# Optimization experiments

Hardware: AMD Instinct MI355X
Metric: run time of the kernel (lower is better)

## Reference

```python
import jax, jax.numpy as jnp
import numpy as np

E = 32      # particle_embed_dim = q/k/v head out dim
G = 2       # nof_net_types (conv groups)
NEG_SLOPE = 0.01


def _glin(x, w, b, groups):
    """Grouped 1x1 conv on (M, C, 1, 1) == grouped linear.
    x: (M, Cin), w: (Cout, Cin//groups), b: (Cout,)."""
    M = x.shape[0]
    Cout = w.shape[0]
    xg = x.reshape(M, groups, -1)                 # (M, G, Cin/G)
    wg = w.reshape(groups, Cout // groups, -1)    # (G, Cout/G, Cin/G)
    y = jnp.einsum('mgi,goi->mgo', xg, wg).reshape(M, Cout)
    return y + b


def setup_inputs() -> dict:
    key = jax.random.key(0)
    ks = jax.random.split(key, 9)
    B, N = 32, 1024
    s = 0.05
    return {
        'x_e':   jax.random.normal(ks[0], (B, N, G * E), dtype=jnp.float32),
        'w_qkv': jax.random.normal(ks[1], (3 * G * E, E), dtype=jnp.float32) * s,
        'b_qkv': jax.random.normal(ks[2], (3 * G * E,), dtype=jnp.float32) * s,
        'w_h1':  jax.random.normal(ks[3], (G * E, 2 * E), dtype=jnp.float32) * s,
        'b_h1':  jax.random.normal(ks[4], (G * E,), dtype=jnp.float32) * s,
        'w_h10': jax.random.normal(ks[5], (G * E, E), dtype=jnp.float32) * s,
        'b_h10': jax.random.normal(ks[6], (G * E,), dtype=jnp.float32) * s,
        'w_h11': jax.random.normal(ks[7], (G * E, E), dtype=jnp.float32) * s,
        'b_h11': jax.random.normal(ks[8], (G * E,), dtype=jnp.float32) * s,
    }


def reference(x_e, w_qkv, b_qkv, w_h1, b_h1, w_h10, b_h10, w_h11, b_h11):
    B, N, D = x_e.shape                      # D = G*E = 64
    act = lambda z: jnp.where(z >= 0, z, NEG_SLOPE * z)

    # grouped 1x1-conv QKV projection
    qkv = _glin(x_e.reshape(B * N, D), w_qkv, b_qkv, G)        # (B*N, 3*G*E)
    qkv = qkv.reshape(B, N, G, 3, E).transpose(0, 2, 3, 1, 4)  # (B, G, 3, N, E)
    q, k, v = qkv[:, :, 0], qkv[:, :, 1], qkv[:, :, 2]         # each (B, G, N, E)

    # NOTE: module divides k by sqrt(E) and logits by sqrt(E) again -> 1/E total
    scale = 1.0 / E
    ip = jnp.einsum('bgne,bgme->bgnm', q, k) * scale           # (B, G, N, N)
    sip = jax.nn.softmax(ip, axis=-1)
    attn = jnp.einsum('bgnm,bgme->bgne', sip, v)               # (B, G, N, E)

    # concat pre-attention v with attention output, regroup per-particle
    x_xe = jnp.concatenate([v, attn], axis=3)                  # (B, G, N, 2E)
    x_xe = x_xe.transpose(0, 2, 1, 3).reshape(B * N, G * 2 * E)  # (B*N, 128)

    h = act(_glin(x_xe, w_h1, b_h1, G))
    h = act(_glin(h, w_h10, b_h10, G))
    h = act(_glin(h, w_h11, b_h11, G))
    return h.reshape(B * N, G * E, 1, 1)
```

## Files before the change

kernel.cpp:

```cpp
#include <hip/hip_runtime.h>

#define B_ 32
#define N_ 1024
#define NEG 0.01f
#define QSC (1.4426950408889634f/32.0f)

using half8  = __attribute__((ext_vector_type(8))) _Float16;
using half4  = __attribute__((ext_vector_type(4))) _Float16;
using half2  = __attribute__((ext_vector_type(2))) _Float16;
using fp16x2 = __attribute__((ext_vector_type(2))) __fp16;
using floatx4 = __attribute__((ext_vector_type(4))) float;

#if defined(__has_builtin)
#if __has_builtin(__builtin_amdgcn_exp2f)
#define EXP2(x) __builtin_amdgcn_exp2f(x)
#endif
#endif
#ifndef EXP2
#define EXP2(x) exp2f(x)
#endif

__device__ inline half2 pkcvt(float a, float b) {
    fp16x2 r = __builtin_amdgcn_cvt_pkrtz(a, b);
    return __builtin_bit_cast(half2, r);
}

__device__ inline half8 cvt8(float4 a, float4 b) {
    half2 p0 = pkcvt(a.x, a.y);
    half2 p1 = pkcvt(a.z, a.w);
    half2 p2 = pkcvt(b.x, b.y);
    half2 p3 = pkcvt(b.z, b.w);
    half8 h = { p0[0],p0[1], p1[0],p1[1], p2[0],p2[1], p3[0],p3[1] };
    return h;
}

struct __align__(16) Smem {
    _Float16 wsh[96*36];
    float    bsh[96];
    _Float16 Kst[2][128*40];
    _Float16 Vtst[2][32*136];
    union {
        _Float16 qs[128*40];
        _Float16 xs[128*72];
    } u;
    float linv[128];
    float bl1[32], bl10[32], bl11[32];
};

__global__ __launch_bounds__(256, 2) void fused_kernel(
    const float* __restrict__ x, const float* __restrict__ w_qkv, const float* __restrict__ b_qkv,
    const float* __restrict__ w_h1,  const float* __restrict__ b_h1,
    const float* __restrict__ w_h10, const float* __restrict__ b_h10,
    const float* __restrict__ w_h11, const float* __restrict__ b_h11,
    float* __restrict__ out)
{
    __shared__ Smem sm;
    int t = threadIdx.x;
    int bg = blockIdx.x >> 3;
    int qtile = blockIdx.x & 7;
    int b = bg >> 1, g = bg & 1;
    int qbase = qtile * 128;
    int lane = t & 63, w = t >> 6;
    int L15 = lane & 15, quad = lane >> 4;

    for (int idx = t; idx < 96*32; idx += 256) {
        int r = idx >> 5, c = idx & 31;
        float wv = w_qkv[(g*96 + r)*32 + c];
        sm.wsh[r*36 + c] = (_Float16)(r < 32 ? wv*QSC : wv);
    }
    if (t < 96) sm.bsh[t] = b_qkv[g*96 + t];
    if (t < 32) {
        sm.bl1[t]  = b_h1[g*32+t];
        sm.bl10[t] = b_h10[g*32+t];
        sm.bl11[t] = b_h11[g*32+t];
    }
    __syncthreads();

    half8 bwq[2], bwk[2], bwv[2];
    floatx4 cq[2], ck[2], cv[2];
    #pragma unroll
    for (int et = 0; et < 2; et++) {
        bwq[et] = *(const half8*)&sm.wsh[(     et*16 + L15)*36 + quad*8];
        bwk[et] = *(const half8*)&sm.wsh[(32 + et*16 + L15)*36 + quad*8];
        bwv[et] = *(const half8*)&sm.wsh[(64 + et*16 + L15)*36 + quad*8];
        float bq = sm.bsh[     et*16 + L15] * QSC;
        float bk = sm.bsh[32 + et*16 + L15];
        float bv = sm.bsh[64 + et*16 + L15];
        cq[et] = (floatx4){bq,bq,bq,bq};
        ck[et] = (floatx4){bk,bk,bk,bk};
        cv[et] = (floatx4){bv,bv,bv,bv};
    }

    {
        floatx4 dq[2][2];
        #pragma unroll
        for (int mt = 0; mt < 2; mt++) {
            const float* p = x + ((size_t)b*N_ + qbase + w*32 + mt*16 + L15)*64 + g*32 + quad*8;
            half8 axq = cvt8(*(const float4*)p, *(const float4*)(p + 4));
            dq[mt][0] = __builtin_amdgcn_mfma_f32_16x16x32_f16(axq, bwq[0], cq[0], 0,0,0);
            dq[mt][1] = __builtin_amdgcn_mfma_f32_16x16x32_f16(axq, bwq[1], cq[1], 0,0,0);
        }
        #pragma unroll
        for (int mt = 0; mt < 2; mt++)
            #pragma unroll
            for (int et = 0; et < 2; et++)
                #pragma unroll
                for (int r = 0; r < 4; r++)
                    sm.u.qs[(w*32 + mt*16 + quad*4 + r)*40 + et*16 + L15] =
                        (_Float16)dq[mt][et][r];
    }
    __syncthreads();
    half8 bq0 = *(const half8*)&sm.u.qs[(w*32 +      L15)*40 + quad*8];
    half8 bq1 = *(const half8*)&sm.u.qs[(w*32 + 16 + L15)*40 + quad*8];

    float4 xf0[2], xf1[2];
    auto prefetch = [&](int tile) {
        #pragma unroll
        for (int mt = 0; mt < 2; mt++) {
            const float* p = x + ((size_t)b*N_ + tile*128 + w*32 + mt*16 + L15)*64 + g*32 + quad*8;
            xf0[mt] = *(const float4*)p;
            xf1[mt] = *(const float4*)(p + 4);
        }
    };
    auto proj_tile = [&](int tile, int buf) {
        floatx4 dK[2][2], dV[2][2];
        #pragma unroll
        for (int mt = 0; mt < 2; mt++) {
            half8 axk = cvt8(xf0[mt], xf1[mt]);
            dK[mt][0] = __builtin_amdgcn_mfma_f32_16x16x32_f16(axk, bwk[0], ck[0], 0,0,0);
            dK[mt][1] = __builtin_amdgcn_mfma_f32_16x16x32_f16(axk, bwk[1], ck[1], 0,0,0);
            dV[mt][0] = __builtin_amdgcn_mfma_f32_16x16x32_f16(axk, bwv[0], cv[0], 0,0,0);
            dV[mt][1] = __builtin_amdgcn_mfma_f32_16x16x32_f16(axk, bwv[1], cv[1], 0,0,0);
        }
        #pragma unroll
        for (int mt = 0; mt < 2; mt++) {
            int rb = w*32 + mt*16 + quad*4;
            #pragma unroll
            for (int et = 0; et < 2; et++) {
                half2 k01 = pkcvt(dK[mt][et][0], dK[mt][et][1]);
                half2 k23 = pkcvt(dK[mt][et][2], dK[mt][et][3]);
                half2 v01 = pkcvt(dV[mt][et][0], dV[mt][et][1]);
                half2 v23 = pkcvt(dV[mt][et][2], dV[mt][et][3]);
                half4 vh = { v01[0], v01[1], v23[0], v23[1] };
                sm.Kst[buf][(rb+0)*40 + et*16 + L15] = k01[0];
                sm.Kst[buf][(rb+1)*40 + et*16 + L15] = k01[1];
                sm.Kst[buf][(rb+2)*40 + et*16 + L15] = k23[0];
                sm.Kst[buf][(rb+3)*40 + et*16 + L15] = k23[1];
                *(half4*)&sm.Vtst[buf][(et*16 + L15)*136 + rb] = vh;
                if (tile == qtile) {
                    #pragma unroll
                    for (int r = 0; r < 4; r++)
                        sm.u.xs[(rb + r)*72 + et*16 + L15] = vh[r];
                }
            }
        }
    };

    prefetch(0);
    proj_tile(0, 0);
    __syncthreads();

    floatx4 o00 = {0.f,0.f,0.f,0.f}, o01 = o00, o10 = o00, o11 = o00;
    float lsum0 = 0.f, lsum1 = 0.f;

    for (int kt = 0; kt < 8; kt++) {
        int cur = kt & 1;
        if (kt < 7) prefetch(kt + 1);
        #pragma unroll
        for (int mt8 = 0; mt8 < 8; mt8++) {
            half8 ak = *(const half8*)&sm.Kst[cur][(mt8*16 + L15)*40 + quad*8];
            floatx4 zz = {0.f,0.f,0.f,0.f};
            floatx4 s0 = __builtin_amdgcn_mfma_f32_16x16x32_f16(ak, bq0, zz, 0,0,0);
            floatx4 s1 = __builtin_amdgcn_mfma_f32_16x16x32_f16(ak, bq1, zz, 0,0,0);
            float p00 = EXP2(s0.x), p01 = EXP2(s0.y), p02 = EXP2(s0.z), p03 = EXP2(s0.w);
            float p10 = EXP2(s1.x), p11 = EXP2(s1.y), p12 = EXP2(s1.z), p13 = EXP2(s1.w);
            lsum0 += (p00+p01)+(p02+p03);
            lsum1 += (p10+p11)+(p12+p13);
            half2 pa = pkcvt(p00, p01);
            half2 pb = pkcvt(p02, p03);
            half2 pc = pkcvt(p10, p11);
            half2 pd = pkcvt(p12, p13);
            half4 a0 = { pa[0], pa[1], pb[0], pb[1] };
            half4 a1 = { pc[0], pc[1], pd[0], pd[1] };
            half4 bv0 = *(const half4*)&sm.Vtst[cur][      L15*136 + mt8*16 + quad*4];
            half4 bv1 = *(const half4*)&sm.Vtst[cur][(16 + L15)*136 + mt8*16 + quad*4];
            o00 = __builtin_amdgcn_mfma_f32_16x16x16f16(a0, bv0, o00, 0,0,0);
            o01 = __builtin_amdgcn_mfma_f32_16x16x16f16(a0, bv1, o01, 0,0,0);
            o10 = __builtin_amdgcn_mfma_f32_16x16x16f16(a1, bv0, o10, 0,0,0);
            o11 = __builtin_amdgcn_mfma_f32_16x16x16f16(a1, bv1, o11, 0,0,0);
        }
        if (kt < 7) proj_tile(kt + 1, 1 - cur);
        __syncthreads();
    }

    lsum0 += __shfl_xor(lsum0, 16, 64); lsum0 += __shfl_xor(lsum0, 32, 64);
    lsum1 += __shfl_xor(lsum1, 16, 64); lsum1 += __shfl_xor(lsum1, 32, 64);
    if (quad == 0) {
        sm.linv[w*32 +      L15] = 1.0f / lsum0;
        sm.linv[w*32 + 16 + L15] = 1.0f / lsum1;
    }
    __syncthreads();

    {
        const floatx4* ofr[2][2] = { {&o00,&o01}, {&o10,&o11} };
        #pragma unroll
        for (int nt = 0; nt < 2; nt++) {
            float4 li = *(const float4*)&sm.linv[w*32 + nt*16 + quad*4];
            #pragma unroll
            for (int et = 0; et < 2; et++) {
                floatx4 ov = *ofr[nt][et];
                sm.u.xs[(w*32+nt*16+quad*4+0)*72 + 32 + et*16 + L15] = (_Float16)(ov[0]*li.x);
                sm.u.xs[(w*32+nt*16+quad*4+1)*72 + 32 + et*16 + L15] = (_Float16)(ov[1]*li.y);
                sm.u.xs[(w*32+nt*16+quad*4+2)*72 + 32 + et*16 + L15] = (_Float16)(ov[2]*li.z);
                sm.u.xs[(w*32+nt*16+quad*4+3)*72 + 32 + et*16 + L15] = (_Float16)(ov[3]*li.w);
            }
        }
    }
    __syncthreads();

    half4 a1f[2][4], a2f[2][2], a3f[2][2];
    #pragma unroll
    for (int mt = 0; mt < 2; mt++) {
        #pragma unroll
        for (int kt = 0; kt < 4; kt++) {
            float4 f = *(const float4*)(w_h1 + (size_t)(g*32+mt*16+L15)*64 + kt*16 + quad*4);
            half2 ha = pkcvt(f.x, f.y);
            half2 hb = pkcvt(f.z, f.w);
            half4 h = { ha[0], ha[1], hb[0], hb[1] };
            a1f[mt][kt] = h;
        }
        #pragma unroll
        for (int kt = 0; kt < 2; kt++) {
            float4 f = *(const float4*)(w_h10 + (size_t)(g*32+mt*16+L15)*32 + kt*16 + quad*4);
            half2 ha = pkcvt(f.x, f.y);
            half2 hb = pkcvt(f.z, f.w);
            half4 h = { ha[0], ha[1], hb[0], hb[1] };
            a2f[mt][kt] = h;
            float4 f2 = *(const float4*)(w_h11 + (size_t)(g*32+mt*16+L15)*32 + kt*16 + quad*4);
            half2 hc = pkcvt(f2.x, f2.y);
            half2 hd = pkcvt(f2.z, f2.w);
            half4 h2 = { hc[0], hc[1], hd[0], hd[1] };
            a3f[mt][kt] = h2;
        }
    }

    floatx4 d1[2][2];
    #pragma unroll
    for (int mt = 0; mt < 2; mt++) {
        float4 bb = *(const float4*)&sm.bl1[mt*16 + quad*4];
        floatx4 seed = { bb.x, bb.y, bb.z, bb.w };
        d1[mt][0] = seed; d1[mt][1] = seed;
    }
    #pragma unroll
    for (int nt = 0; nt < 2; nt++)
        #pragma unroll
        for (int kt = 0; kt < 4; kt++) {
            half4 b1 = *(const half4*)&sm.u.xs[(w*32+nt*16+L15)*72 + kt*16 + quad*4];
            d1[0][nt] = __builtin_amdgcn_mfma_f32_16x16x16f16(a1f[0][kt], b1, d1[0][nt], 0,0,0);
            d1[1][nt] = __builtin_amdgcn_mfma_f32_16x16x16f16(a1f[1][kt], b1, d1[1][nt], 0,0,0);
        }
    half4 h1b[2][2];
    #pragma unroll
    for (int mt = 0; mt < 2; mt++)
        #pragma unroll
        for (int nt = 0; nt < 2; nt++) {
            float v0 = d1[mt][nt][0]; v0 = (v0>=0.f)?v0:NEG*v0;
            float v1 = d1[mt][nt][1]; v1 = (v1>=0.f)?v1:NEG*v1;
            float v2 = d1[mt][nt][2]; v2 = (v2>=0.f)?v2:NEG*v2;
            float v3 = d1[mt][nt][3]; v3 = (v3>=0.f)?v3:NEG*v3;
            half2 ha = pkcvt(v0, v1);
            half2 hb = pkcvt(v2, v3);
            half4 h = { ha[0], ha[1], hb[0], hb[1] };
            h1b[mt][nt] = h;
        }
    floatx4 d2[2][2];
    #pragma unroll
    for (int mt = 0; mt < 2; mt++) {
        float4 bb = *(const float4*)&sm.bl10[mt*16 + quad*4];
        floatx4 seed = { bb.x, bb.y, bb.z, bb.w };
        d2[mt][0] = seed; d2[mt][1] = seed;
    }
    #pragma unroll
    for (int mt = 0; mt < 2; mt++)
        #pragma unroll
        for (int nt = 0; nt < 2; nt++)
            #pragma unroll
            for (int kt = 0; kt < 2; kt++)
                d2[mt][nt] = __builtin_amdgcn_mfma_f32_16x16x16f16(a2f[mt][kt], h1b[kt][nt], d2[mt][nt], 0,0,0);
    half4 h2b[2][2];
    #pragma unroll
    for (int mt = 0; mt < 2; mt++)
        #pragma unroll
        for (int nt = 0; nt < 2; nt++) {
            float v0 = d2[mt][nt][0]; v0 = (v0>=0.f)?v0:NEG*v0;
            float v1 = d2[mt][nt][1]; v1 = (v1>=0.f)?v1:NEG*v1;
            float v2 = d2[mt][nt][2]; v2 = (v2>=0.f)?v2:NEG*v2;
            float v3 = d2[mt][nt][3]; v3 = (v3>=0.f)?v3:NEG*v3;
            half2 ha = pkcvt(v0, v1);
            half2 hb = pkcvt(v2, v3);
            half4 h = { ha[0], ha[1], hb[0], hb[1] };
            h2b[mt][nt] = h;
        }
    floatx4 d3[2][2];
    #pragma unroll
    for (int mt = 0; mt < 2; mt++) {
        float4 bb = *(const float4*)&sm.bl11[mt*16 + quad*4];
        floatx4 seed = { bb.x, bb.y, bb.z, bb.w };
        d3[mt][0] = seed; d3[mt][1] = seed;
    }
    #pragma unroll
    for (int mt = 0; mt < 2; mt++)
        #pragma unroll
        for (int nt = 0; nt < 2; nt++)
            #pragma unroll
            for (int kt = 0; kt < 2; kt++)
                d3[mt][nt] = __builtin_amdgcn_mfma_f32_16x16x16f16(a3f[mt][kt], h2b[kt][nt], d3[mt][nt], 0,0,0);
    #pragma unroll
    for (int mt = 0; mt < 2; mt++)
        #pragma unroll
        for (int nt = 0; nt < 2; nt++) {
            float4 ov;
            ov.x = d3[mt][nt][0]; ov.x = (ov.x>=0.f)?ov.x:NEG*ov.x;
            ov.y = d3[mt][nt][1]; ov.y = (ov.y>=0.f)?ov.y:NEG*ov.y;
            ov.z = d3[mt][nt][2]; ov.z = (ov.z>=0.f)?ov.z:NEG*ov.z;
            ov.w = d3[mt][nt][3]; ov.w = (ov.w>=0.f)?ov.w:NEG*ov.w;
            *(float4*)(out + ((size_t)b*N_ + qbase + w*32 + nt*16 + L15)*64 + g*32 + mt*16 + quad*4) = ov;
        }
}

extern "C" void kernel_launch(void* const* d_in, const int* in_sizes, int n_in,
                              void* d_out, int out_size, void* d_ws, size_t ws_size,
                              hipStream_t stream) {
    const float* x_e   = (const float*)d_in[0];
    const float* w_qkv = (const float*)d_in[1];
    const float* b_qkv = (const float*)d_in[2];
    const float* w_h1  = (const float*)d_in[3];
    const float* b_h1  = (const float*)d_in[4];
    const float* w_h10 = (const float*)d_in[5];
    const float* b_h10 = (const float*)d_in[6];
    const float* w_h11 = (const float*)d_in[7];
    const float* b_h11 = (const float*)d_in[8];
    float* out = (float*)d_out;

    hipLaunchKernelGGL(fused_kernel, dim3(B_*2*8), dim3(256), 0, stream,
                       x_e, w_qkv, b_qkv, w_h1, b_h1, w_h10, b_h10, w_h11, b_h11, out);
}
```

Measured before the change: 98.32 us.

## Use 512-thread blocks with 16 query rows per wave and XCD-aware block mapping

Doubles the block to 8 waves so each wave owns 16 query rows instead of 32. This halves per-wave register state (one score MFMA per K subtile, two output accumulators) and raises occupancy through launch bounds 512,4. Block IDs are remapped so all query tiles of one batch-group land on the same XCD, improving L2 reuse of the shared K/V input. It also raises MFMA priority with s_setprio around the attention loop and replaces the shared-memory linv round-trip plus two barriers with wave shuffles. In exchange, the K/V projection is still recomputed per block and more waves contend at each barrier.

Result: slower. 150.2 us (+52.7%).

```diff
diff --git a/kernel.cpp b/kernel.cpp
--- a/kernel.cpp
+++ b/kernel.cpp
@@ -20,6 +20,9 @@
 #define EXP2(x) exp2f(x)
 #endif
 
+#define MFMA32 __builtin_amdgcn_mfma_f32_16x16x32_f16
+#define MFMA16 __builtin_amdgcn_mfma_f32_16x16x16f16
+
 __device__ inline half2 pkcvt(float a, float b) {
     fp16x2 r = __builtin_amdgcn_cvt_pkrtz(a, b);
     return __builtin_bit_cast(half2, r);
@@ -39,15 +42,12 @@
     float    bsh[96];
     _Float16 Kst[2][128*40];
     _Float16 Vtst[2][32*136];
-    union {
-        _Float16 qs[128*40];
-        _Float16 xs[128*72];
-    } u;
-    float linv[128];
+    _Float16 qs[128*40];
+    _Float16 xs[128*72];
     float bl1[32], bl10[32], bl11[32];
 };
 
-__global__ __launch_bounds__(256, 2) void fused_kernel(
+__global__ __launch_bounds__(512, 4) void fused_kernel(
     const float* __restrict__ x, const float* __restrict__ w_qkv, const float* __restrict__ b_qkv,
     const float* __restrict__ w_h1,  const float* __restrict__ b_h1,
     const float* __restrict__ w_h10, const float* __restrict__ b_h10,
@@ -56,14 +56,16 @@
 {
     __shared__ Smem sm;
     int t = threadIdx.x;
-    int bg = blockIdx.x >> 3;
-    int qtile = blockIdx.x & 7;
+    int bid = blockIdx.x;
+    int xcd = bid & 7, j = bid >> 3;
+    int bg = xcd*8 + (j >> 3);
+    int qtile = j & 7;
     int b = bg >> 1, g = bg & 1;
     int qbase = qtile * 128;
     int lane = t & 63, w = t >> 6;
     int L15 = lane & 15, quad = lane >> 4;
 
-    for (int idx = t; idx < 96*32; idx += 256) {
+    for (int idx = t; idx < 96*32; idx += 512) {
         int r = idx >> 5, c = idx & 31;
         float wv = w_qkv[(g*96 + r)*32 + c];
         sm.wsh[r*36 + c] = (_Float16)(r < 32 ? wv*QSC : wv);
@@ -76,82 +78,66 @@
     }
     __syncthreads();
 
-    half8 bwq[2], bwk[2], bwv[2];
-    floatx4 cq[2], ck[2], cv[2];
+    half8 bwk[2], bwv[2];
+    float bkv[2], bvv[2];
     #pragma unroll
     for (int et = 0; et < 2; et++) {
-        bwq[et] = *(const half8*)&sm.wsh[(     et*16 + L15)*36 + quad*8];
         bwk[et] = *(const half8*)&sm.wsh[(32 + et*16 + L15)*36 + quad*8];
         bwv[et] = *(const half8*)&sm.wsh[(64 + et*16 + L15)*36 + quad*8];
-        float bq = sm.bsh[     et*16 + L15] * QSC;
-        float bk = sm.bsh[32 + et*16 + L15];
-        float bv = sm.bsh[64 + et*16 + L15];
-        cq[et] = (floatx4){bq,bq,bq,bq};
-        ck[et] = (floatx4){bk,bk,bk,bk};
-        cv[et] = (floatx4){bv,bv,bv,bv};
+        bkv[et] = sm.bsh[32 + et*16 + L15];
+        bvv[et] = sm.bsh[64 + et*16 + L15];
     }
 
     {
-        floatx4 dq[2][2];
-        #pragma unroll
-        for (int mt = 0; mt < 2; mt++) {
-            const float* p = x + ((size_t)b*N_ + qbase + w*32 + mt*16 + L15)*64 + g*32 + quad*8;
-            half8 axq = cvt8(*(const float4*)p, *(const float4*)(p + 4));
-            dq[mt][0] = __builtin_amdgcn_mfma_f32_16x16x32_f16(axq, bwq[0], cq[0], 0,0,0);
-            dq[mt][1] = __builtin_amdgcn_mfma_f32_16x16x32_f16(axq, bwq[1], cq[1], 0,0,0);
-        }
-        #pragma unroll
-        for (int mt = 0; mt < 2; mt++)
+        const float* p = x + ((size_t)b*N_ + qbase + w*16 + L15)*64 + g*32 + quad*8;
+        half8 axq = cvt8(*(const float4*)p, *(const float4*)(p + 4));
+        #pragma unroll
+        for (int et = 0; et < 2; et++) {
+            half8 bwq = *(const half8*)&sm.wsh[(et*16 + L15)*36 + quad*8];
+            float bq = sm.bsh[et*16 + L15] * QSC;
+            floatx4 cq = {bq,bq,bq,bq};
+            floatx4 dq = MFMA32(axq, bwq, cq, 0,0,0);
             #pragma unroll
-            for (int et = 0; et < 2; et++)
+            for (int r = 0; r < 4; r++)
+                sm.qs[(w*16 + quad*4 + r)*40 + et*16 + L15] = (_Float16)dq[r];
+        }
+    }
+    __syncthreads();
+    half8 bq0 = *(const half8*)&sm.qs[(w*16 + L15)*40 + quad*8];
+
+    float4 xf0, xf1;
+    auto prefetch = [&](int tile) {
+        const float* p = x + ((size_t)b*N_ + tile*128 + w*16 + L15)*64 + g*32 + quad*8;
+        xf0 = *(const float4*)p;
+        xf1 = *(const float4*)(p + 4);
+    };
+    auto proj_tile = [&](int tile, int buf) {
+        half8 ax = cvt8(xf0, xf1);
+        floatx4 dK[2], dV[2];
+        #pragma unroll
+        for (int et = 0; et < 2; et++) {
+            floatx4 ck = {bkv[et],bkv[et],bkv[et],bkv[et]};
+            floatx4 cv = {bvv[et],bvv[et],bvv[et],bvv[et]};
+            dK[et] = MFMA32(ax, bwk[et], ck, 0,0,0);
+            dV[et] = MFMA32(ax, bwv[et], cv, 0,0,0);
+        }
+        int rb = w*16 + quad*4;
+        #pragma unroll
+        for (int et = 0; et < 2; et++) {
+            half2 k01 = pkcvt(dK[et][0], dK[et][1]);
+            half2 k23 = pkcvt(dK[et][2], dK[et][3]);
+            sm.Kst[buf][(rb+0)*40 + et*16 + L15] = k01[0];
+            sm.Kst[buf][(rb+1)*40 + et*16 + L15] = k01[1];
+            sm.Kst[buf][(rb+2)*40 + et*16 + L15] = k23[0];
+            sm.Kst[buf][(rb+3)*40 + et*16 + L15] = k23[1];
+            half2 v01 = pkcvt(dV[et][0], dV[et][1]);
+            half2 v23 = pkcvt(dV[et][2], dV[et][3]);
+            half4 vh = { v01[0], v01[1], v23[0], v23[1] };
+            *(half4*)&sm.Vtst[buf][(et*16 + L15)*136 + rb] = vh;
+            if (tile == qtile) {
                 #pragma unroll
                 for (int r = 0; r < 4; r++)
-                    sm.u.qs[(w*32 + mt*16 + quad*4 + r)*40 + et*16 + L15] =
-                        (_Float16)dq[mt][et][r];
-    }
-    __syncthreads();
-    half8 bq0 = *(const half8*)&sm.u.qs[(w*32 +      L15)*40 + quad*8];
-    half8 bq1 = *(const half8*)&sm.u.qs[(w*32 + 16 + L15)*40 + quad*8];
-
-    float4 xf0[2], xf1[2];
-    auto prefetch = [&](int tile) {
-        #pragma unroll
-        for (int mt = 0; mt < 2; mt++) {
-            const float* p = x + ((size_t)b*N_ + tile*128 + w*32 + mt*16 + L15)*64 + g*32 + quad*8;
-            xf0[mt] = *(const float4*)p;
-            xf1[mt] = *(const float4*)(p + 4);
-        }
-    };
-    auto proj_tile = [&](int tile, int buf) {
-        floatx4 dK[2][2], dV[2][2];
-        #pragma unroll
-        for (int mt = 0; mt < 2; mt++) {
-            half8 axk = cvt8(xf0[mt], xf1[mt]);
-            dK[mt][0] = __builtin_amdgcn_mfma_f32_16x16x32_f16(axk, bwk[0], ck[0], 0,0,0);
-            dK[mt][1] = __builtin_amdgcn_mfma_f32_16x16x32_f16(axk, bwk[1], ck[1], 0,0,0);
-            dV[mt][0] = __builtin_amdgcn_mfma_f32_16x16x32_f16(axk, bwv[0], cv[0], 0,0,0);
-            dV[mt][1] = __builtin_amdgcn_mfma_f32_16x16x32_f16(axk, bwv[1], cv[1], 0,0,0);
-        }
-        #pragma unroll
-        for (int mt = 0; mt < 2; mt++) {
-            int rb = w*32 + mt*16 + quad*4;
-            #pragma unroll
-            for (int et = 0; et < 2; et++) {
-                half2 k01 = pkcvt(dK[mt][et][0], dK[mt][et][1]);
-                half2 k23 = pkcvt(dK[mt][et][2], dK[mt][et][3]);
-                half2 v01 = pkcvt(dV[mt][et][0], dV[mt][et][1]);
-                half2 v23 = pkcvt(dV[mt][et][2], dV[mt][et][3]);
-                half4 vh = { v01[0], v01[1], v23[0], v23[1] };
-                sm.Kst[buf][(rb+0)*40 + et*16 + L15] = k01[0];
-                sm.Kst[buf][(rb+1)*40 + et*16 + L15] = k01[1];
-                sm.Kst[buf][(rb+2)*40 + et*16 + L15] = k23[0];
-                sm.Kst[buf][(rb+3)*40 + et*16 + L15] = k23[1];
-                *(half4*)&sm.Vtst[buf][(et*16 + L15)*136 + rb] = vh;
-                if (tile == qtile) {
-                    #pragma unroll
-                    for (int r = 0; r < 4; r++)
-                        sm.u.xs[(rb + r)*72 + et*16 + L15] = vh[r];
-                }
+                    sm.xs[(rb + r)*72 + et*16 + L15] = vh[r];
             }
         }
     };
@@ -160,63 +146,51 @@
     proj_tile(0, 0);
     __syncthreads();
 
-    floatx4 o00 = {0.f,0.f,0.f,0.f}, o01 = o00, o10 = o00, o11 = o00;
-    float lsum0 = 0.f, lsum1 = 0.f;
+    const floatx4 zz = {0.f,0.f,0.f,0.f};
+    floatx4 o00 = zz, o01 = zz;
+    float lsum0 = 0.f;
 
     for (int kt = 0; kt < 8; kt++) {
         int cur = kt & 1;
         if (kt < 7) prefetch(kt + 1);
-        #pragma unroll
-        for (int mt8 = 0; mt8 < 8; mt8++) {
-            half8 ak = *(const half8*)&sm.Kst[cur][(mt8*16 + L15)*40 + quad*8];
-            floatx4 zz = {0.f,0.f,0.f,0.f};
-            floatx4 s0 = __builtin_amdgcn_mfma_f32_16x16x32_f16(ak, bq0, zz, 0,0,0);
-            floatx4 s1 = __builtin_amdgcn_mfma_f32_16x16x32_f16(ak, bq1, zz, 0,0,0);
+        __builtin_amdgcn_s_setprio(1);
+        #pragma unroll
+        for (int m8 = 0; m8 < 8; m8++) {
+            half8 ak = *(const half8*)&sm.Kst[cur][(m8*16 + L15)*40 + quad*8];
+            floatx4 s0 = MFMA32(ak, bq0, zz, 0,0,0);
             float p00 = EXP2(s0.x), p01 = EXP2(s0.y), p02 = EXP2(s0.z), p03 = EXP2(s0.w);
-            float p10 = EXP2(s1.x), p11 = EXP2(s1.y), p12 = EXP2(s1.z), p13 = EXP2(s1.w);
             lsum0 += (p00+p01)+(p02+p03);
-            lsum1 += (p10+p11)+(p12+p13);
             half2 pa = pkcvt(p00, p01);
             half2 pb = pkcvt(p02, p03);
-            half2 pc = pkcvt(p10, p11);
-            half2 pd = pkcvt(p12, p13);
             half4 a0 = { pa[0], pa[1], pb[0], pb[1] };
-            half4 a1 = { pc[0], pc[1], pd[0], pd[1] };
-            half4 bv0 = *(const half4*)&sm.Vtst[cur][      L15*136 + mt8*16 + quad*4];
-            half4 bv1 = *(const half4*)&sm.Vtst[cur][(16 + L15)*136 + mt8*16 + quad*4];
-            o00 = __builtin_amdgcn_mfma_f32_16x16x16f16(a0, bv0, o00, 0,0,0);
-            o01 = __builtin_amdgcn_mfma_f32_16x16x16f16(a0, bv1, o01, 0,0,0);
-            o10 = __builtin_amdgcn_mfma_f32_16x16x16f16(a1, bv0, o10, 0,0,0);
-            o11 = __builtin_amdgcn_mfma_f32_16x16x16f16(a1, bv1, o11, 0,0,0);
-        }
-        if (kt < 7) proj_tile(kt + 1, 1 - cur);
-        __syncthreads();
-    }
-
-    lsum0 += __shfl_xor(lsum0, 16, 64); lsum0 += __shfl_xor(lsum0, 32, 64);
-    lsum1 += __shfl_xor(lsum1, 16, 64); lsum1 += __shfl_xor(lsum1, 32, 64);
-    if (quad == 0) {
-        sm.linv[w*32 +      L15] = 1.0f / lsum0;
-        sm.linv[w*32 + 16 + L15] = 1.0f / lsum1;
-    }
-    __syncthreads();
-
-    {
-        const floatx4* ofr[2][2] = { {&o00,&o01}, {&o10,&o11} };
-        #pragma unroll
-        for (int nt = 0; nt < 2; nt++) {
-            float4 li = *(const float4*)&sm.linv[w*32 + nt*16 + quad*4];
-            #pragma unroll
-            for (int et = 0; et < 2; et++) {
-                floatx4 ov = *ofr[nt][et];
-                sm.u.xs[(w*32+nt*16+quad*4+0)*72 + 32 + et*16 + L15] = (_Float16)(ov[0]*li.x);
-                sm.u.xs[(w*32+nt*16+quad*4+1)*72 + 32 + et*16 + L15] = (_Float16)(ov[1]*li.y);
-                sm.u.xs[(w*32+nt*16+quad*4+2)*72 + 32 + et*16 + L15] = (_Float16)(ov[2]*li.z);
-                sm.u.xs[(w*32+nt*16+quad*4+3)*72 + 32 + et*16 + L15] = (_Float16)(ov[3]*li.w);
-            }
-        }
-    }
-    __syncthreads();
+            half4 bv0 = *(const half4*)&sm.Vtst[cur][      L15*136 + m8*16 + quad*4];
+            half4 bv1 = *(const half4*)&sm.Vtst[cur][(16 + L15)*136 + m8*16 + quad*4];
+            o00 = MFMA16(a0, bv0, o00, 0,0,0);
+            o01 = MFMA16(a0, bv1, o01, 0,0,0);
+        }
+        __builtin_amdgcn_s_setprio(0);
+        if (kt < 7) {
+            proj_tile(kt + 1, 1 - cur);
+            __syncthreads();
+        }
+    }
+
+    lsum0 += __shfl_xor(lsum0, 16, 64);
+    lsum0 += __shfl_xor(lsum0, 32, 64);
+    float linv_own = 1.0f / lsum0;
+    float li0 = __shfl(linv_own, quad*4 + 0, 64);
+    float li1 = __shfl(linv_own, quad*4 + 1, 64);
+    float li2 = __shfl(linv_own, quad*4 + 2, 64);
+    float li3 = __shfl(linv_own, quad*4 + 3, 64);
+
+    #pragma unroll
+    for (int et = 0; et < 2; et++) {
+        floatx4 ov = et ? o01 : o00;
+        sm.xs[(w*16+quad*4+0)*72 + 32 + et*16 + L15] = (_Float16)(ov[0]*li0);
+        sm.xs[(w*16+quad*4+1)*72 + 32 + et*16 + L15] = (_Float16)(ov[1]*li1);
+        sm.xs[(w*16+quad*4+2)*72 + 32 + et*16 + L15] = (_Float16)(ov[2]*li2);
+        sm.xs[(w*16+quad*4+3)*72 + 32 + et*16 + L15] = (_Float16)(ov[3]*li3);
+    }
 
     half4 a1f[2][4], a2f[2][2], a3f[2][2];
     #pragma unroll
@@ -226,16 +200,16 @@
             float4 f = *(const float4*)(w_h1 + (size_t)(g*32+mt*16+L15)*64 + kt*16 + quad*4);
             half2 ha = pkcvt(f.x, f.y);
             half2 hb = pkcvt(f.z, f.w);
-            half4 h = { ha[0], ha[1], hb[0], hb[1] };
-            a1f[mt][kt] = h;
+            half4 hh = { ha[0], ha[1], hb[0], hb[1] };
+            a1f[mt][kt] = hh;
         }
         #pragma unroll
         for (int kt = 0; kt < 2; kt++) {
             float4 f = *(const float4*)(w_h10 + (size_t)(g*32+mt*16+L15)*32 + kt*16 + quad*4);
             half2 ha = pkcvt(f.x, f.y);
             half2 hb = pkcvt(f.z, f.w);
-            half4 h = { ha[0], ha[1], hb[0], hb[1] };
-            a2f[mt][kt] = h;
+            half4 hh = { ha[0], ha[1], hb[0], hb[1] };
+            a2f[mt][kt] = hh;
             float4 f2 = *(const float4*)(w_h11 + (size_t)(g*32+mt*16+L15)*32 + kt*16 + quad*4);
             half2 hc = pkcvt(f2.x, f2.y);
             half2 hd = pkcvt(f2.z, f2.w);
@@ -244,88 +218,69 @@
         }
     }
 
-    floatx4 d1[2][2];
+    floatx4 d1[2];
     #pragma unroll
     for (int mt = 0; mt < 2; mt++) {
         float4 bb = *(const float4*)&sm.bl1[mt*16 + quad*4];
-        floatx4 seed = { bb.x, bb.y, bb.z, bb.w };
-        d1[mt][0] = seed; d1[mt][1] = seed;
-    }
-    #pragma unroll
-    for (int nt = 0; nt < 2; nt++)
-        #pragma unroll
-        for (int kt = 0; kt < 4; kt++) {
-            half4 b1 = *(const half4*)&sm.u.xs[(w*32+nt*16+L15)*72 + kt*16 + quad*4];
-            d1[0][nt] = __builtin_amdgcn_mfma_f32_16x16x16f16(a1f[0][kt], b1, d1[0][nt], 0,0,0);
-            d1[1][nt] = __builtin_amdgcn_mfma_f32_16x16x16f16(a1f[1][kt], b1, d1[1][nt], 0,0,0);
-        }
-    half4 h1b[2][2];
-    #pragma unroll
-    for (int mt = 0; mt < 2; mt++)
-        #pragma unroll
-        for (int nt = 0; nt < 2; nt++) {
-            float v0 = d1[mt][nt][0]; v0 = (v0>=0.f)?v0:NEG*v0;
-            float v1 = d1[mt][nt][1]; v1 = (v1>=0.f)?v1:NEG*v1;
-            float v2 = d1[mt][nt][2]; v2 = (v2>=0.f)?v2:NEG*v2;
-            float v3 = d1[mt][nt][3]; v3 = (v3>=0.f)?v3:NEG*v3;
-            half2 ha = pkcvt(v0, v1);
-            half2 hb = pkcvt(v2, v3);
-            half4 h = { ha[0], ha[1], hb[0], hb[1] };
-            h1b[mt][nt] = h;
-        }
-    floatx4 d2[2][2];
+        d1[mt] = (floatx4){bb.x, bb.y, bb.z, bb.w};
+    }
+    #pragma unroll
+    for (int kt = 0; kt < 4; kt++) {
+        half4 b1 = *(const half4*)&sm.xs[(w*16 + L15)*72 + kt*16 + quad*4];
+        d1[0] = MFMA16(a1f[0][kt], b1, d1[0], 0,0,0);
+        d1[1] = MFMA16(a1f[1][kt], b1, d1[1], 0,0,0);
+    }
+    half4 h1b[2];
+    #pragma unroll
+    for (int mt = 0; mt < 2; mt++) {
+        float v0 = d1[mt][0]; v0 = (v0>=0.f)?v0:NEG*v0;
+        float v1 = d1[mt][1]; v1 = (v1>=0.f)?v1:NEG*v1;
+        float v2 = d1[mt][2]; v2 = (v2>=0.f)?v2:NEG*v2;
+        float v3 = d1[mt][3]; v3 = (v3>=0.f)?v3:NEG*v3;
+        half2 ha = pkcvt(v0, v1);
+        half2 hb = pkcvt(v2, v3);
+        half4 hh = { ha[0], ha[1], hb[0], hb[1] };
+        h1b[mt] = hh;
+    }
+    floatx4 d2[2];
     #pragma unroll
     for (int mt = 0; mt < 2; mt++) {
         float4 bb = *(const float4*)&sm.bl10[mt*16 + quad*4];
-        floatx4 seed = { bb.x, bb.y, bb.z, bb.w };
-        d2[mt][0] = seed; d2[mt][1] = seed;
-    }
-    #pragma unroll
-    for (int mt = 0; mt < 2; mt++)
-        #pragma unroll
-        for (int nt = 0; nt < 2; nt++)
-            #pragma unroll
-            for (int kt = 0; kt < 2; kt++)
-                d2[mt][nt] = __builtin_amdgcn_mfma_f32_16x16x16f16(a2f[mt][kt], h1b[kt][nt], d2[mt][nt], 0,0,0);
-    half4 h2b[2][2];
-    #pragma unroll
-    for (int mt = 0; mt < 2; mt++)
-        #pragma unroll
-        for (int nt = 0; nt < 2; nt++) {
-            float v0 = d2[mt][nt][0]; v0 = (v0>=0.f)?v0:NEG*v0;
-            float v1 = d2[mt][nt][1]; v1 = (v1>=0.f)?v1:NEG*v1;
-            float v2 = d2[mt][nt][2]; v2 = (v2>=0.f)?v2:NEG*v2;
-            float v3 = d2[mt][nt][3]; v3 = (v3>=0.f)?v3:NEG*v3;
-            half2 ha = pkcvt(v0, v1);
-            half2 hb = pkcvt(v2, v3);
-            half4 h = { ha[0], ha[1], hb[0], hb[1] };
-            h2b[mt][nt] = h;
-        }
-    floatx4 d3[2][2];
+        d2[mt] = (floatx4){bb.x, bb.y, bb.z, bb.w};
+        #pragma unroll
+        for (int kt = 0; kt < 2; kt++)
+            d2[mt] = MFMA16(a2f[mt][kt], h1b[kt], d2[mt], 0,0,0);
+    }
+    half4 h2b[2];
+    #pragma unroll
+    for (int mt = 0; mt < 2; mt++) {
+        float v0 = d2[mt][0]; v0 = (v0>=0.f)?v0:NEG*v0;
+        float v1 = d2[mt][1]; v1 = (v1>=0.f)?v1:NEG*v1;
+        float v2 = d2[mt][2]; v2 = (v2>=0.f)?v2:NEG*v2;
+        float v3 = d2[mt][3]; v3 = (v3>=0.f)?v3:NEG*v3;
+        half2 ha = pkcvt(v0, v1);
+        half2 hb = pkcvt(v2, v3);
+        half4 hh = { ha[0], ha[1], hb[0], hb[1] };
+        h2b[mt] = hh;
+    }
+    floatx4 d3[2];
     #pragma unroll
     for (int mt = 0; mt < 2; mt++) {
         float4 bb = *(const float4*)&sm.bl11[mt*16 + quad*4];
-        floatx4 seed = { bb.x, bb.y, bb.z, bb.w };
-        d3[mt][0] = seed; d3[mt][1] = seed;
-    }
-    #pragma unroll
-    for (int mt = 0; mt < 2; mt++)
-        #pragma unroll
-        for (int nt = 0; nt < 2; nt++)
-            #pragma unroll
-            for (int kt = 0; kt < 2; kt++)
-                d3[mt][nt] = __builtin_amdgcn_mfma_f32_16x16x16f16(a3f[mt][kt], h2b[kt][nt], d3[mt][nt], 0,0,0);
-    #pragma unroll
-    for (int mt = 0; mt < 2; mt++)
-        #pragma unroll
-        for (int nt = 0; nt < 2; nt++) {
-            float4 ov;
-            ov.x = d3[mt][nt][0]; ov.x = (ov.x>=0.f)?ov.x:NEG*ov.x;
-            ov.y = d3[mt][nt][1]; ov.y = (ov.y>=0.f)?ov.y:NEG*ov.y;
-            ov.z = d3[mt][nt][2]; ov.z = (ov.z>=0.f)?ov.z:NEG*ov.z;
-            ov.w = d3[mt][nt][3]; ov.w = (ov.w>=0.f)?ov.w:NEG*ov.w;
-            *(float4*)(out + ((size_t)b*N_ + qbase + w*32 + nt*16 + L15)*64 + g*32 + mt*16 + quad*4) = ov;
-        }
+        d3[mt] = (floatx4){bb.x, bb.y, bb.z, bb.w};
+        #pragma unroll
+        for (int kt = 0; kt < 2; kt++)
+            d3[mt] = MFMA16(a3f[mt][kt], h2b[kt], d3[mt], 0,0,0);
+    }
+    #pragma unroll
+    for (int mt = 0; mt < 2; mt++) {
+        float4 ov;
+        ov.x = d3[mt][0]; ov.x = (ov.x>=0.f)?ov.x:NEG*ov.x;
+        ov.y = d3[mt][1]; ov.y = (ov.y>=0.f)?ov.y:NEG*ov.y;
+        ov.z = d3[mt][2]; ov.z = (ov.z>=0.f)?ov.z:NEG*ov.z;
+        ov.w = d3[mt][3]; ov.w = (ov.w>=0.f)?ov.w:NEG*ov.w;
+        *(float4*)(out + ((size_t)b*N_ + qbase + w*16 + L15)*64 + g*32 + mt*16 + quad*4) = ov;
+    }
 }
 
 extern "C" void kernel_launch(void* const* d_in, const int* in_sizes, int n_in,
@@ -342,6 +297,6 @@
     const float* b_h11 = (const float*)d_in[8];
     float* out = (float*)d_out;
 
-    hipLaunchKernelGGL(fused_kernel, dim3(B_*2*8), dim3(256), 0, stream,
+    hipLaunchKernelGGL(fused_kernel, dim3(B_*2*8), dim3(512), 0, stream,
                        x_e, w_qkv, b_qkv, w_h1, b_h1, w_h10, b_h10, w_h11, b_h11, out);
 }
```

## Remap blocks per XCD, raise MFMA priority, and drop barriers via shuffles

Applied to the files above, without the earlier changes.

Block IDs are remapped so that the eight query tiles of one (batch, group) pair land on the same XCD, which is meant to improve L2 reuse of the shared x rows. The attention inner loop now raises wave priority with s_setprio around the MFMA/exp section. The softmax row normalisers are broadcast with lane shuffles instead of an LDS array, which removes one barrier; the barrier after the last tile and the one before the MLP are also dropped. A new barrier is added after reading Q from the union buffer, so the xs writes in proj_tile can no longer overwrite qs while other waves are still reading it. Each wave appears to read back only its own xs rows in the MLP stage, which would make the dropped barriers safe.

Result: no change. 97.86 us (-0.5%).

```diff
diff --git a/kernel.cpp b/kernel.cpp
--- a/kernel.cpp
+++ b/kernel.cpp
@@ -19,6 +19,9 @@
 #ifndef EXP2
 #define EXP2(x) exp2f(x)
 #endif
+
+#define MFMA32 __builtin_amdgcn_mfma_f32_16x16x32_f16
+#define MFMA16 __builtin_amdgcn_mfma_f32_16x16x16f16
 
 __device__ inline half2 pkcvt(float a, float b) {
     fp16x2 r = __builtin_amdgcn_cvt_pkrtz(a, b);
@@ -43,7 +46,6 @@
         _Float16 qs[128*40];
         _Float16 xs[128*72];
     } u;
-    float linv[128];
     float bl1[32], bl10[32], bl11[32];
 };
 
@@ -56,8 +58,10 @@
 {
     __shared__ Smem sm;
     int t = threadIdx.x;
-    int bg = blockIdx.x >> 3;
-    int qtile = blockIdx.x & 7;
+    int bid = blockIdx.x;
+    int xcd = bid & 7, j = bid >> 3;
+    int bg = xcd*8 + (j >> 3);
+    int qtile = j & 7;
     int b = bg >> 1, g = bg & 1;
     int qbase = qtile * 128;
     int lane = t & 63, w = t >> 6;
@@ -97,8 +101,8 @@
         for (int mt = 0; mt < 2; mt++) {
             const float* p = x + ((size_t)b*N_ + qbase + w*32 + mt*16 + L15)*64 + g*32 + quad*8;
             half8 axq = cvt8(*(const float4*)p, *(const float4*)(p + 4));
-            dq[mt][0] = __builtin_amdgcn_mfma_f32_16x16x32_f16(axq, bwq[0], cq[0], 0,0,0);
-            dq[mt][1] = __builtin_amdgcn_mfma_f32_16x16x32_f16(axq, bwq[1], cq[1], 0,0,0);
+            dq[mt][0] = MFMA32(axq, bwq[0], cq[0], 0,0,0);
+            dq[mt][1] = MFMA32(axq, bwq[1], cq[1], 0,0,0);
         }
         #pragma unroll
         for (int mt = 0; mt < 2; mt++)
@@ -112,6 +116,7 @@
     __syncthreads();
     half8 bq0 = *(const half8*)&sm.u.qs[(w*32 +      L15)*40 + quad*8];
     half8 bq1 = *(const half8*)&sm.u.qs[(w*32 + 16 + L15)*40 + quad*8];
+    __syncthreads();
 
     float4 xf0[2], xf1[2];
     auto prefetch = [&](int tile) {
@@ -127,10 +132,10 @@
         #pragma unroll
         for (int mt = 0; mt < 2; mt++) {
             half8 axk = cvt8(xf0[mt], xf1[mt]);
-            dK[mt][0] = __builtin_amdgcn_mfma_f32_16x16x32_f16(axk, bwk[0], ck[0], 0,0,0);
-            dK[mt][1] = __builtin_amdgcn_mfma_f32_16x16x32_f16(axk, bwk[1], ck[1], 0,0,0);
-            dV[mt][0] = __builtin_amdgcn_mfma_f32_16x16x32_f16(axk, bwv[0], cv[0], 0,0,0);
-            dV[mt][1] = __builtin_amdgcn_mfma_f32_16x16x32_f16(axk, bwv[1], cv[1], 0,0,0);
+            dK[mt][0] = MFMA32(axk, bwk[0], ck[0], 0,0,0);
+            dK[mt][1] = MFMA32(axk, bwk[1], ck[1], 0,0,0);
+            dV[mt][0] = MFMA32(axk, bwv[0], cv[0], 0,0,0);
+            dV[mt][1] = MFMA32(axk, bwv[1], cv[1], 0,0,0);
         }
         #pragma unroll
         for (int mt = 0; mt < 2; mt++) {
@@ -166,12 +171,13 @@
     for (int kt = 0; kt < 8; kt++) {
         int cur = kt & 1;
         if (kt < 7) prefetch(kt + 1);
+        __builtin_amdgcn_s_setprio(1);
         #pragma unroll
         for (int mt8 = 0; mt8 < 8; mt8++) {
             half8 ak = *(const half8*)&sm.Kst[cur][(mt8*16 + L15)*40 + quad*8];
             floatx4 zz = {0.f,0.f,0.f,0.f};
-            floatx4 s0 = __builtin_amdgcn_mfma_f32_16x16x32_f16(ak, bq0, zz, 0,0,0);
-            floatx4 s1 = __builtin_amdgcn_mfma_f32_16x16x32_f16(ak, bq1, zz, 0,0,0);
+            floatx4 s0 = MFMA32(ak, bq0, zz, 0,0,0);
+            floatx4 s1 = MFMA32(ak, bq1, zz, 0,0,0);
             float p00 = EXP2(s0.x), p01 = EXP2(s0.y), p02 = EXP2(s0.z), p03 = EXP2(s0.w);
             float p10 = EXP2(s1.x), p11 = EXP2(s1.y), p12 = EXP2(s1.z), p13 = EXP2(s1.w);
             lsum0 += (p00+p01)+(p02+p03);
@@ -184,39 +190,43 @@
             half4 a1 = { pc[0], pc[1], pd[0], pd[1] };
             half4 bv0 = *(const half4*)&sm.Vtst[cur][      L15*136 + mt8*16 + quad*4];
             half4 bv1 = *(const half4*)&sm.Vtst[cur][(16 + L15)*136 + mt8*16 + quad*4];
-            o00 = __builtin_amdgcn_mfma_f32_16x16x16f16(a0, bv0, o00, 0,0,0);
-            o01 = __builtin_amdgcn_mfma_f32_16x16x16f16(a0, bv1, o01, 0,0,0);
-            o10 = __builtin_amdgcn_mfma_f32_16x16x16f16(a1, bv0, o10, 0,0,0);
-            o11 = __builtin_amdgcn_mfma_f32_16x16x16f16(a1, bv1, o11, 0,0,0);
-        }
-        if (kt < 7) proj_tile(kt + 1, 1 - cur);
-        __syncthreads();
+            o00 = MFMA16(a0, bv0, o00, 0,0,0);
+            o01 = MFMA16(a0, bv1, o01, 0,0,0);
+            o10 = MFMA16(a1, bv0, o10, 0,0,0);
+            o11 = MFMA16(a1, bv1, o11, 0,0,0);
+        }
+        __builtin_amdgcn_s_setprio(0);
+        if (kt < 7) {
+            proj_tile(kt + 1, 1 - cur);
+            __syncthreads();
+        }
     }
 
     lsum0 += __shfl_xor(lsum0, 16, 64); lsum0 += __shfl_xor(lsum0, 32, 64);
     lsum1 += __shfl_xor(lsum1, 16, 64); lsum1 += __shfl_xor(lsum1, 32, 64);
-    if (quad == 0) {
-        sm.linv[w*32 +      L15] = 1.0f / lsum0;
-        sm.linv[w*32 + 16 + L15] = 1.0f / lsum1;
-    }
-    __syncthreads();
+    float inv0 = 1.0f / lsum0;
+    float inv1 = 1.0f / lsum1;
+    float li[2][4];
+    #pragma unroll
+    for (int r = 0; r < 4; r++) {
+        li[0][r] = __shfl(inv0, quad*4 + r, 64);
+        li[1][r] = __shfl(inv1, quad*4 + r, 64);
+    }
 
     {
         const floatx4* ofr[2][2] = { {&o00,&o01}, {&o10,&o11} };
         #pragma unroll
         for (int nt = 0; nt < 2; nt++) {
-            float4 li = *(const float4*)&sm.linv[w*32 + nt*16 + quad*4];
             #pragma unroll
             for (int et = 0; et < 2; et++) {
                 floatx4 ov = *ofr[nt][et];
-                sm.u.xs[(w*32+nt*16+quad*4+0)*72 + 32 + et*16 + L15] = (_Float16)(ov[0]*li.x);
-                sm.u.xs[(w*32+nt*16+quad*4+1)*72 + 32 + et*16 + L15] = (_Float16)(ov[1]*li.y);
-                sm.u.xs[(w*32+nt*16+quad*4+2)*72 + 32 + et*16 + L15] = (_Float16)(ov[2]*li.z);
-                sm.u.xs[(w*32+nt*16+quad*4+3)*72 + 32 + et*16 + L15] = (_Float16)(ov[3]*li.w);
+                sm.u.xs[(w*32+nt*16+quad*4+0)*72 + 32 + et*16 + L15] = (_Float16)(ov[0]*li[nt][0]);
+                sm.u.xs[(w*32+nt*16+quad*4+1)*72 + 32 + et*16 + L15] = (_Float16)(ov[1]*li[nt][1]);
+                sm.u.xs[(w*32+nt*16+quad*4+2)*72 + 32 + et*16 + L15] = (_Float16)(ov[2]*li[nt][2]);
+                sm.u.xs[(w*32+nt*16+quad*4+3)*72 + 32 + et*16 + L15] = (_Float16)(ov[3]*li[nt][3]);
             }
         }
     }
-    __syncthreads();
 
     half4 a1f[2][4], a2f[2][2], a3f[2][2];
     #pragma unroll
@@ -256,8 +266,8 @@
         #pragma unroll
         for (int kt = 0; kt < 4; kt++) {
             half4 b1 = *(const half4*)&sm.u.xs[(w*32+nt*16+L15)*72 + kt*16 + quad*4];
-            d1[0][nt] = __builtin_amdgcn_mfma_f32_16x16x16f16(a1f[0][kt], b1, d1[0][nt], 0,0,0);
-            d1[1][nt] = __builtin_amdgcn_mfma_f32_16x16x16f16(a1f[1][kt], b1, d1[1][nt], 0,0,0);
+            d1[0][nt] = MFMA16(a1f[0][kt], b1, d1[0][nt], 0,0,0);
+            d1[1][nt] = MFMA16(a1f[1][kt], b1, d1[1][nt], 0,0,0);
         }
     half4 h1b[2][2];
     #pragma unroll
@@ -286,7 +296,7 @@
         for (int nt = 0; nt < 2; nt++)
             #pragma unroll
             for (int kt = 0; kt < 2; kt++)
-                d2[mt][nt] = __builtin_amdgcn_mfma_f32_16x16x16f16(a2f[mt][kt], h1b[kt][nt], d2[mt][nt], 0,0,0);
+                d2[mt][nt] = MFMA16(a2f[mt][kt], h1b[kt][nt], d2[mt][nt], 0,0,0);
     half4 h2b[2][2];
     #pragma unroll
     for (int mt = 0; mt < 2; mt++)
@@ -314,7 +324,7 @@
         for (int nt = 0; nt < 2; nt++)
             #pragma unroll
             for (int kt = 0; kt < 2; kt++)
-                d3[mt][nt] = __builtin_amdgcn_mfma_f32_16x16x16f16(a3f[mt][kt], h2b[kt][nt], d3[mt][nt], 0,0,0);
+                d3[mt][nt] = MFMA16(a3f[mt][kt], h2b[kt][nt], d3[mt][nt], 0,0,0);
     #pragma unroll
     for (int mt = 0; mt < 2; mt++)
         #pragma unroll
```
